# Optimization experiments

Measured on AMD Instinct MI355X. Metric: run time of the kernel, lower is better.

Reference implementation:

```python
import jax, jax.numpy as jnp
import numpy as np

B, S, F = 512, 512, 128   # batch, seq_len, facts_size (= querry_size)
H1, H2 = 80, 40
PAD = float(-2**32 + 1)


def setup_inputs() -> dict:
    key = jax.random.key(0)
    ks = jax.random.split(key, 12)
    inp = {
        "query": jax.random.normal(ks[0], (B, F), jnp.float32),
        "facts": jax.random.normal(ks[1], (B, S, F), jnp.float32),
        "mask": jax.random.randint(ks[2], (B, S), 0, 2, jnp.int32),
        # mlp1: querry_size -> facts_size
        "W1": jax.random.normal(ks[3], (F, F), jnp.float32) / np.sqrt(F),
        "b1": jnp.zeros((F,), jnp.float32),
        # PReLU alpha (per-feature, init zeros)
        "alpha": jnp.zeros((F,), jnp.float32),
        # mlp2: 4*F -> 80
        "W2": jax.random.normal(ks[4], (4 * F, H1), jnp.float32) / np.sqrt(4 * F),
        "b2": jnp.zeros((H1,), jnp.float32),
        # mlp3: 80 -> 40
        "W3": jax.random.normal(ks[5], (H1, H2), jnp.float32) / np.sqrt(H1),
        "b3": jnp.zeros((H2,), jnp.float32),
        # mlp4: 40 -> 1
        "W4": jax.random.normal(ks[6], (H2, 1), jnp.float32) / np.sqrt(H2),
        "b4": jnp.zeros((1,), jnp.float32),
    }
    return inp


def reference(query, facts, mask, W1, b1, alpha, W2, b2, W3, b3, W4, b4):
    # mlp1 + PReLU on the query
    q = query @ W1 + b1                                   # [B, F]
    q = jnp.where(q >= 0, q, alpha * q)                   # PReLU, alpha per-feature
    # broadcast query over sequence (tile+reshape in the original)
    qs = jnp.broadcast_to(q[:, None, :], (q.shape[0], S, F))  # [B, S, F]
    din = jnp.concatenate([qs, facts, qs - facts, qs * facts], axis=-1)  # [B,S,4F]
    h1 = jax.nn.sigmoid(din @ W2 + b2)                    # [B, S, 80]
    h2 = jax.nn.sigmoid(h1 @ W3 + b3)                     # [B, S, 40]
    scores = (h2 @ W4 + b4)[..., 0][:, None, :]           # [B, 1, S]
    key_masks = (mask == 1)[:, None, :]                   # [B, 1, S]
    scores = jnp.where(key_masks, scores, PAD)
    scores = jax.nn.softmax(scores, axis=-1)              # softmax over seq
    out = jnp.einsum("bqs,bsf->bqf", scores, facts)       # [B, 1, F]  (mode SUM)
    return out
```

## Files before the change

kernel.cpp:

```cpp
#include <hip/hip_runtime.h>
#include <hip/hip_bf16.h>

typedef __bf16 bf16x8 __attribute__((ext_vector_type(8)));
typedef float  f32x4  __attribute__((ext_vector_type(4)));

#define WBT_STRIDE 136
#define H1_STRIDE  104
#define W3T_STRIDE 104

__global__ __launch_bounds__(512, 4)
void attn_fused(const float* __restrict__ query,
                const float* __restrict__ facts,
                const int*   __restrict__ mask,
                const float* __restrict__ W1, const float* __restrict__ b1,
                const float* __restrict__ alpha,
                const float* __restrict__ W2, const float* __restrict__ b2,
                const float* __restrict__ W3, const float* __restrict__ b3,
                const float* __restrict__ W4,
                float* __restrict__ out)
{
    __shared__ __align__(16) __bf16 WbT[80 * WBT_STRIDE];
    __shared__ __align__(16) __bf16 W3T[48 * W3T_STRIDE];
    __shared__ __align__(16) __bf16 h1all[128 * H1_STRIDE];
    __shared__ float qy[128], qs[128], qcs[80];
    __shared__ float qpart[4][128], qcp[4][80];
    __shared__ float w4s[48], b3s[48];
    __shared__ float outw[8 * 128];
    __shared__ float Zw[8];

    const int b = blockIdx.x, t = threadIdx.x;
    const int wave = t >> 6, lane = t & 63, qd = lane >> 4, m = lane & 15;
    const float* fb = facts + (size_t)b * (512 * 128);
    const int*   mb = mask + b * 512;

    f32x4 av[2][4][2];
    int mv[4];
    {
        const float* p0 = &fb[(size_t)(wave * 64 + m) * 128 + qd * 8];
        #pragma unroll
        for (int kc = 0; kc < 4; ++kc) {
            av[0][kc][0] = *(const f32x4*)(p0 + kc * 32);
            av[0][kc][1] = *(const f32x4*)(p0 + kc * 32 + 4);
        }
        #pragma unroll
        for (int tl = 0; tl < 4; ++tl) mv[tl] = mb[wave * 64 + tl * 16 + m];
    }

    if (t < 128) qy[t] = query[b * 128 + t];
    for (int e = t; e < 48 * 96; e += 512) {
        int j = e / 96, k = e % 96;
        W3T[j * W3T_STRIDE + k] = (j < 40 && k < 80) ? (__bf16)W3[k * 40 + j]
                                                     : (__bf16)0.0f;
    }
    for (int e = t; e < 128 * 16; e += 512) {
        int r = e >> 4, c = 80 + (e & 15);
        h1all[r * H1_STRIDE + c] = (__bf16)0.0f;
    }
    if (t < 48) { w4s[t] = (t < 40) ? W4[t] : 0.f; b3s[t] = (t < 40) ? b3[t] : 0.f; }
    __syncthreads();

    {
        int j = t & 127, kh = t >> 7;
        float acc = (kh == 0) ? b1[j] : 0.f;
        const float* w1p = W1 + (kh * 32) * 128 + j;
        #pragma unroll 8
        for (int k = 0; k < 32; ++k) acc = fmaf(qy[kh * 32 + k], w1p[k * 128], acc);
        qpart[kh][j] = acc;
    }
    __syncthreads();
    if (t < 128) {
        float s = (qpart[0][t] + qpart[1][t]) + (qpart[2][t] + qpart[3][t]);
        qs[t] = (s >= 0.f) ? s : alpha[t] * s;
    }
    __syncthreads();

    if (t < 320) {
        int jj = t % 80, hh = t / 80;
        float acc = (hh == 0) ? b2[jj] : 0.f;
        #pragma unroll 8
        for (int k = hh * 32; k < hh * 32 + 32; ++k)
            acc = fmaf(qs[k], W2[k * 80 + jj] + W2[(256 + k) * 80 + jj], acc);
        qcp[hh][jj] = acc;
    }
    for (int e = t; e < 128 * 80; e += 512) {
        int k = e / 80, n = e - k * 80;
        float w = W2[(128 + k) * 80 + n] - W2[(256 + k) * 80 + n]
                + qs[k] * W2[(384 + k) * 80 + n];
        WbT[n * WBT_STRIDE + (((k >> 3) ^ (n & 3)) << 3) + (k & 7)] = (__bf16)w;
    }
    __syncthreads();
    if (t < 80) qcs[t] = (qcp[0][t] + qcp[1][t]) + (qcp[2][t] + qcp[3][t]);
    __syncthreads();

    __bf16* h1w = &h1all[wave * 16 * H1_STRIDE];

    float oacc[4][8];
    #pragma unroll
    for (int kc = 0; kc < 4; ++kc)
        #pragma unroll
        for (int i = 0; i < 8; ++i) oacc[kc][i] = 0.f;
    float Zl = 0.f;
    float pmprev = 0.f;

    #pragma unroll
    for (int tile = 0; tile < 4; ++tile) {
        const int p = tile & 1;

        if (tile > 0) {
            #pragma unroll
            for (int kc = 0; kc < 4; ++kc)
                #pragma unroll
                for (int i = 0; i < 4; ++i) {
                    oacc[kc][i]     = fmaf(pmprev, av[1 - p][kc][0][i], oacc[kc][i]);
                    oacc[kc][i + 4] = fmaf(pmprev, av[1 - p][kc][1][i], oacc[kc][i + 4]);
                }
            Zl += pmprev;
        }
        if (tile < 3) {
            const float* pn = &fb[(size_t)(wave * 64 + (tile + 1) * 16 + m) * 128 + qd * 8];
            #pragma unroll
            for (int kc = 0; kc < 4; ++kc) {
                av[1 - p][kc][0] = *(const f32x4*)(pn + kc * 32);
                av[1 - p][kc][1] = *(const f32x4*)(pn + kc * 32 + 4);
            }
        }

        bf16x8 af[4];
        #pragma unroll
        for (int kc = 0; kc < 4; ++kc)
            #pragma unroll
            for (int i = 0; i < 8; ++i)
                af[kc][i] = (__bf16)((i < 4) ? av[p][kc][0][i] : av[p][kc][1][i - 4]);

        #pragma unroll
        for (int ct = 0; ct < 5; ++ct) {
            f32x4 acc = {0.f, 0.f, 0.f, 0.f};
            const int n1 = ct * 16 + m;
            #pragma unroll
            for (int kc = 0; kc < 4; ++kc) {
                bf16x8 bfr = *(const bf16x8*)
                    &WbT[n1 * WBT_STRIDE + (((kc * 4 + qd) ^ (m & 3)) << 3)];
                acc = __builtin_amdgcn_mfma_f32_16x16x32_bf16(af[kc], bfr, acc, 0, 0, 0);
            }
            const float qc = qcs[n1];
            #pragma unroll
            for (int r = 0; r < 4; ++r) {
                float x = acc[r] + qc;
                float h = __builtin_amdgcn_rcpf(1.0f + __expf(-x));
                h1w[(qd * 4 + r) * H1_STRIDE + n1] = (__bf16)h;
            }
        }
        asm volatile("s_waitcnt lgkmcnt(0)" ::: "memory");

        bf16x8 a2[3];
        #pragma unroll
        for (int kc = 0; kc < 3; ++kc)
            a2[kc] = *(const bf16x8*)&h1w[m * H1_STRIDE + kc * 32 + qd * 8];
        float sc[4] = {0.f, 0.f, 0.f, 0.f};
        #pragma unroll
        for (int ct = 0; ct < 3; ++ct) {
            f32x4 acc2 = {0.f, 0.f, 0.f, 0.f};
            #pragma unroll
            for (int kc = 0; kc < 3; ++kc) {
                bf16x8 bfr = *(const bf16x8*)&W3T[(ct * 16 + m) * W3T_STRIDE + kc * 32 + qd * 8];
                acc2 = __builtin_amdgcn_mfma_f32_16x16x32_bf16(a2[kc], bfr, acc2, 0, 0, 0);
            }
            const int col = ct * 16 + m;
            const float w4v = w4s[col], b3v = b3s[col];
            #pragma unroll
            for (int r = 0; r < 4; ++r) {
                float h2 = __builtin_amdgcn_rcpf(1.0f + __expf(-(acc2[r] + b3v)));
                sc[r] = fmaf(h2, w4v, sc[r]);
            }
        }
        #pragma unroll
        for (int d = 1; d < 16; d <<= 1)
            #pragma unroll
            for (int r = 0; r < 4; ++r)
                sc[r] += __shfl_xor(sc[r], d);

        const int idx = ((((m >> 2) << 4) | m) << 2);
        float s0v = __int_as_float(__builtin_amdgcn_ds_bpermute(idx, __float_as_int(sc[0])));
        float s1v = __int_as_float(__builtin_amdgcn_ds_bpermute(idx, __float_as_int(sc[1])));
        float s2v = __int_as_float(__builtin_amdgcn_ds_bpermute(idx, __float_as_int(sc[2])));
        float s3v = __int_as_float(__builtin_amdgcn_ds_bpermute(idx, __float_as_int(sc[3])));
        const int rr = m & 3;
        float srow = (rr == 0) ? s0v : (rr == 1) ? s1v : (rr == 2) ? s2v : s3v;

        pmprev = (mv[tile] == 1) ? __expf(srow) : 0.f;
    }
    #pragma unroll
    for (int kc = 0; kc < 4; ++kc)
        #pragma unroll
        for (int i = 0; i < 4; ++i) {
            oacc[kc][i]     = fmaf(pmprev, av[1][kc][0][i], oacc[kc][i]);
            oacc[kc][i + 4] = fmaf(pmprev, av[1][kc][1][i], oacc[kc][i + 4]);
        }
    Zl += pmprev;

    #pragma unroll
    for (int d = 1; d < 16; d <<= 1) {
        #pragma unroll
        for (int kc = 0; kc < 4; ++kc)
            #pragma unroll
            for (int i = 0; i < 8; ++i)
                oacc[kc][i] += __shfl_xor(oacc[kc][i], d);
        Zl += __shfl_xor(Zl, d);
    }
    if (m == 0) {
        #pragma unroll
        for (int kc = 0; kc < 4; ++kc)
            #pragma unroll
            for (int i = 0; i < 8; ++i)
                outw[wave * 128 + kc * 32 + qd * 8 + i] = oacc[kc][i];
        if (lane == 0) Zw[wave] = Zl;
    }
    __syncthreads();

    if (t < 128) {
        float v = 0.f, Z = 0.f;
        #pragma unroll
        for (int w = 0; w < 8; ++w) { v += outw[w * 128 + t]; Z += Zw[w]; }
        out[b * 128 + t] = v / Z;
    }
}

extern "C" void kernel_launch(void* const* d_in, const int* in_sizes, int n_in,
                              void* d_out, int out_size, void* d_ws, size_t ws_size,
                              hipStream_t stream) {
    (void)in_sizes; (void)n_in; (void)d_ws; (void)ws_size; (void)out_size;
    const float* query = (const float*)d_in[0];
    const float* facts = (const float*)d_in[1];
    const int*   mask  = (const int*)d_in[2];
    const float* W1 = (const float*)d_in[3];
    const float* b1 = (const float*)d_in[4];
    const float* al = (const float*)d_in[5];
    const float* W2 = (const float*)d_in[6];
    const float* b2 = (const float*)d_in[7];
    const float* W3 = (const float*)d_in[8];
    const float* b3 = (const float*)d_in[9];
    const float* W4 = (const float*)d_in[10];
    const float* b4 = (const float*)d_in[11];
    (void)b4;
    attn_fused<<<dim3(512), dim3(512), 0, stream>>>(
        query, facts, mask, W1, b1, al, W2, b2, W3, b3, W4, (float*)d_out);
}
```

Before: 248.5 us.

## Replace register-held softmax accumulation with score staging and facts re-read

Per-row exp scores now go to shared memory instead of being folded into 32 register accumulators while the MLP tiles run. Afterwards each wave re-reads its 64 facts rows from global memory with coalesced float2 loads to form the weighted sum, which drops the long cross-lane shuffle reduction and frees registers. The price is a second read of the facts (likely served from cache) and an extra barrier. The XOR swizzle on the WbT shared layout is also removed, which may bring back LDS bank conflicts on the B-fragment loads.

```diff
diff --git a/kernel.cpp b/kernel.cpp
--- a/kernel.cpp
+++ b/kernel.cpp
@@ -3,6 +3,7 @@
 
 typedef __bf16 bf16x8 __attribute__((ext_vector_type(8)));
 typedef float  f32x4  __attribute__((ext_vector_type(4)));
+typedef float  f32x2  __attribute__((ext_vector_type(2)));
 
 #define WBT_STRIDE 136
 #define H1_STRIDE  104
@@ -25,7 +26,7 @@
     __shared__ float qy[128], qs[128], qcs[80];
     __shared__ float qpart[4][128], qcp[4][80];
     __shared__ float w4s[48], b3s[48];
-    __shared__ float outw[8 * 128];
+    __shared__ float scores[512];
     __shared__ float Zw[8];
 
     const int b = blockIdx.x, t = threadIdx.x;
@@ -86,36 +87,18 @@
         int k = e / 80, n = e - k * 80;
         float w = W2[(128 + k) * 80 + n] - W2[(256 + k) * 80 + n]
                 + qs[k] * W2[(384 + k) * 80 + n];
-        WbT[n * WBT_STRIDE + (((k >> 3) ^ (n & 3)) << 3) + (k & 7)] = (__bf16)w;
+        WbT[n * WBT_STRIDE + k] = (__bf16)w;
     }
     __syncthreads();
     if (t < 80) qcs[t] = (qcp[0][t] + qcp[1][t]) + (qcp[2][t] + qcp[3][t]);
     __syncthreads();
 
     __bf16* h1w = &h1all[wave * 16 * H1_STRIDE];
-
-    float oacc[4][8];
-    #pragma unroll
-    for (int kc = 0; kc < 4; ++kc)
-        #pragma unroll
-        for (int i = 0; i < 8; ++i) oacc[kc][i] = 0.f;
-    float Zl = 0.f;
-    float pmprev = 0.f;
 
     #pragma unroll
     for (int tile = 0; tile < 4; ++tile) {
         const int p = tile & 1;
 
-        if (tile > 0) {
-            #pragma unroll
-            for (int kc = 0; kc < 4; ++kc)
-                #pragma unroll
-                for (int i = 0; i < 4; ++i) {
-                    oacc[kc][i]     = fmaf(pmprev, av[1 - p][kc][0][i], oacc[kc][i]);
-                    oacc[kc][i + 4] = fmaf(pmprev, av[1 - p][kc][1][i], oacc[kc][i + 4]);
-                }
-            Zl += pmprev;
-        }
         if (tile < 3) {
             const float* pn = &fb[(size_t)(wave * 64 + (tile + 1) * 16 + m) * 128 + qd * 8];
             #pragma unroll
@@ -138,8 +121,7 @@
             const int n1 = ct * 16 + m;
             #pragma unroll
             for (int kc = 0; kc < 4; ++kc) {
-                bf16x8 bfr = *(const bf16x8*)
-                    &WbT[n1 * WBT_STRIDE + (((kc * 4 + qd) ^ (m & 3)) << 3)];
+                bf16x8 bfr = *(const bf16x8*)&WbT[n1 * WBT_STRIDE + kc * 32 + qd * 8];
                 acc = __builtin_amdgcn_mfma_f32_16x16x32_bf16(af[kc], bfr, acc, 0, 0, 0);
             }
             const float qc = qcs[n1];
@@ -187,41 +169,39 @@
         const int rr = m & 3;
         float srow = (rr == 0) ? s0v : (rr == 1) ? s1v : (rr == 2) ? s2v : s3v;
 
-        pmprev = (mv[tile] == 1) ? __expf(srow) : 0.f;
-    }
+        const float pm = (mv[tile] == 1) ? __expf(srow) : 0.f;
+        if (lane < 16) scores[wave * 64 + tile * 16 + lane] = pm;
+    }
+    __syncthreads();
+
+    float z = scores[t];
     #pragma unroll
-    for (int kc = 0; kc < 4; ++kc)
-        #pragma unroll
-        for (int i = 0; i < 4; ++i) {
-            oacc[kc][i]     = fmaf(pmprev, av[1][kc][0][i], oacc[kc][i]);
-            oacc[kc][i + 4] = fmaf(pmprev, av[1][kc][1][i], oacc[kc][i + 4]);
-        }
-    Zl += pmprev;
-
-    #pragma unroll
-    for (int d = 1; d < 16; d <<= 1) {
-        #pragma unroll
-        for (int kc = 0; kc < 4; ++kc)
-            #pragma unroll
-            for (int i = 0; i < 8; ++i)
-                oacc[kc][i] += __shfl_xor(oacc[kc][i], d);
-        Zl += __shfl_xor(Zl, d);
-    }
-    if (m == 0) {
-        #pragma unroll
-        for (int kc = 0; kc < 4; ++kc)
-            #pragma unroll
-            for (int i = 0; i < 8; ++i)
-                outw[wave * 128 + kc * 32 + qd * 8 + i] = oacc[kc][i];
-        if (lane == 0) Zw[wave] = Zl;
-    }
+    for (int d = 1; d < 64; d <<= 1) z += __shfl_xor(z, d);
+    if (lane == 0) Zw[wave] = z;
+
+    float a0 = 0.f, a1 = 0.f;
+    {
+        const float* rp = fb + (size_t)(wave * 64) * 128 + 2 * lane;
+        const float* pp = &scores[wave * 64];
+        #pragma unroll 8
+        for (int s = 0; s < 64; ++s) {
+            f32x2 v = *(const f32x2*)(rp + (size_t)s * 128);
+            const float p = pp[s];
+            a0 = fmaf(p, v[0], a0);
+            a1 = fmaf(p, v[1], a1);
+        }
+    }
+    float* outw = (float*)h1all;
+    __syncthreads();
+    outw[wave * 128 + 2 * lane]     = a0;
+    outw[wave * 128 + 2 * lane + 1] = a1;
     __syncthreads();
 
     if (t < 128) {
-        float v = 0.f, Z = 0.f;
-        #pragma unroll
-        for (int w = 0; w < 8; ++w) { v += outw[w * 128 + t]; Z += Zw[w]; }
-        out[b * 128 + t] = v / Z;
+        float Zg = 0.f, v = 0.f;
+        #pragma unroll
+        for (int w = 0; w < 8; ++w) { v += outw[w * 128 + t]; Zg += Zw[w]; }
+        out[b * 128 + t] = v / Zg;
     }
 }
 
```

New measurement: 234.2 us. 5.7% less time.
